# Kernel optimization log

Measured on AMD Instinct MI355X. Metric: run time of the kernel, lower is better.

The kernel has to match this reference:

```python
import jax, jax.numpy as jnp
import numpy as np

B, T, C, H, W = 8, 8, 32, 16, 28
NH, DK = 4, 8                 # n_head, d_k == d_v
RADIUS = [3, 3, 3, 3]
DILATION = [1, 3, 5, 7]
LN_EPS = 1e-5


def setup_inputs() -> dict:
    key = jax.random.key(0)
    ks = jax.random.split(key, 8)
    s = 1.0 / np.sqrt(C).astype(np.float32)
    return {
        "first": jax.random.normal(ks[0], (B, T, C, H, W), jnp.float32),
        "x": jax.random.normal(ks[1], (B, T, C, H, W), jnp.float32),
        "Wq": jax.random.normal(ks[2], (NH * DK, C), jnp.float32) * s,
        "Wk": jax.random.normal(ks[3], (NH * DK, C), jnp.float32) * s,
        "Wv": jax.random.normal(ks[4], (NH * DK, C), jnp.float32) * s,
        "Wo": jax.random.normal(ks[5], (C, NH * DK), jnp.float32) * s,
        "ln_gamma": 1.0 + 0.1 * jax.random.normal(ks[6], (DK, H, W), jnp.float32),
        "ln_beta": 0.1 * jax.random.normal(ks[7], (DK, H, W), jnp.float32),
    }


def _shift(x, dy, dx):
    # out[..., i, j] = x[..., i+dy, j+dx]; zero out-of-bounds. mask: (H, W) valid.
    h, w = x.shape[-2:]
    xs = jnp.roll(x, (-dy, -dx), axis=(-2, -1))
    mh = (jnp.arange(h) + dy >= 0) & (jnp.arange(h) + dy < h)
    mw = (jnp.arange(w) + dx >= 0) & (jnp.arange(w) + dx < w)
    m = mh[:, None] & mw[None, :]
    return jnp.where(m, xs, 0.0), m


def _head_attn(q, k, v, radius, dilation, scale):
    # q,k,v: (b,t,c,h,w). Returns softmaxed scores P (b,t,O*t,h,w) and
    # aggregation T (b,t,c,h,w). Aggregation uses RAW scaled scores (as the repo
    # does: spatial_temporal_aggregation receives M_A_i, not its softmax).
    b, t, c, h, w = q.shape
    scores, vals, masks = [], [], []
    for dy in range(-radius, radius + 1):
        for dx in range(-radius, radius + 1):
            ks, m = _shift(k, dy * dilation, dx * dilation)
            vs, _ = _shift(v, dy * dilation, dx * dilation)
            # score against all source frames s at the shifted spatial location
            scores.append(jnp.einsum('btchw,bschw->btshw', q, ks))
            vals.append(vs)
            masks.append(m)
    A = jnp.stack(scores, axis=2)                      # (b,t,O,s,h,w), O=(2r+1)^2
    M = jnp.stack(masks, axis=0)                       # (O,h,w)
    A = jnp.where(M[None, None, :, None], A / scale, -jnp.inf)
    O = A.shape[2]
    P = jax.nn.softmax(A.reshape(b, t, O * t, h, w), axis=2)
    Wm = jnp.where(M[None, None, :, None], A, 0.0)     # skip invalid (-inf) slots
    V = jnp.stack(vals, axis=0)                        # (O,b,s,c,h,w)
    Tout = jnp.einsum('btoshw,obschw->btchw', Wm, V)
    return P, Tout


def reference(first, x, Wq, Wk, Wv, Wo, ln_gamma, ln_beta):
    b, t, c, h, w = x.shape
    q = jnp.einsum('btchw,oc->btohw', first, Wq).reshape(b, t, NH, DK, h, w)
    k = jnp.einsum('btchw,oc->btohw', x, Wk).reshape(b, t, NH, DK, h, w)
    v = jnp.einsum('btchw,oc->btohw', x, Wv).reshape(b, t, NH, DK, h, w)
    scale = float(np.sqrt(C / NH))
    Ps, Ts = [], []
    for i in range(NH):
        qi = q[:, :, i]
        mu = jnp.mean(qi, axis=(2, 3, 4), keepdims=True)
        var = jnp.var(qi, axis=(2, 3, 4), keepdims=True)
        qi = (qi - mu) / jnp.sqrt(var + LN_EPS) * ln_gamma + ln_beta
        P, Ti = _head_attn(qi, k[:, :, i], v[:, :, i], RADIUS[i], DILATION[i], scale)
        Ps.append(P)
        Ts.append(Ti)
    M_S = jnp.max(jnp.concatenate(Ps, axis=2), axis=2)   # (b,t,h,w)
    M_T = jnp.concatenate(Ts, axis=2)                    # (b,t,NH*DK,h,w)
    out = jnp.einsum('btchw,oc->btohw', M_T, Wo) * M_S[:, :, None]
    return out
```

## Files before the change

kernel.cpp:

```cpp
#include <hip/hip_runtime.h>

#define Bc 8
#define Tc 8
#define Cc 32
#define Hc 16
#define Wc 28
#define NHc 4
#define DKc 8
#define HWc (Hc*Wc)
#define INV_SCALE 0.35355339059327373f
#define LN_EPSc 1e-5f

typedef _Float16 half8 __attribute__((ext_vector_type(8)));


__global__ __launch_bounds__(448) void qkv_ln_kernel(
    const float* __restrict__ first, const float* __restrict__ x,
    const float* __restrict__ Wq, const float* __restrict__ Wk,
    const float* __restrict__ Wv,
    const float* __restrict__ gamma, const float* __restrict__ beta,
    float4* __restrict__ Q, float* __restrict__ K, float* __restrict__ V)
{
    int blk  = blockIdx.x;
    int head = blk >> 6;
    int bt   = blk & 63;
    int t    = bt % Tc;
    int b    = bt / Tc;
    int tid  = threadIdx.x;

    const float* fp = first + (size_t)bt * Cc * HWc + tid;
    const float* xp = x     + (size_t)bt * Cc * HWc + tid;
    float fv[Cc], xv[Cc];
#pragma unroll
    for (int c = 0; c < Cc; ++c) { fv[c] = fp[c*HWc]; xv[c] = xp[c*HWc]; }

    float qv[DKc], kv[DKc], vv[DKc];
#pragma unroll
    for (int dk = 0; dk < DKc; ++dk) {
        int o = head*DKc + dk;
        float aq = 0.f, ak = 0.f, av = 0.f;
#pragma unroll
        for (int c = 0; c < Cc; ++c) {
            aq = fmaf(Wq[o*Cc+c], fv[c], aq);
            ak = fmaf(Wk[o*Cc+c], xv[c], ak);
            av = fmaf(Wv[o*Cc+c], xv[c], av);
        }
        qv[dk] = aq; kv[dk] = ak; vv[dk] = av;
    }

    int bh = b*NHc + head;
    float* kp = K + (((size_t)bh*Tc + t)*HWc + tid)*DKc;
    float* vp = V + (((size_t)bh*Tc + t)*HWc + tid)*DKc;
    *(float4*)(kp)   = make_float4(kv[0],kv[1],kv[2],kv[3]);
    *(float4*)(kp+4) = make_float4(kv[4],kv[5],kv[6],kv[7]);
    *(float4*)(vp)   = make_float4(vv[0],vv[1],vv[2],vv[3]);
    *(float4*)(vp+4) = make_float4(vv[4],vv[5],vv[6],vv[7]);

    float s1 = 0.f, s2 = 0.f;
#pragma unroll
    for (int dk = 0; dk < DKc; ++dk) { s1 += qv[dk]; s2 += qv[dk]*qv[dk]; }
#pragma unroll
    for (int off = 32; off >= 1; off >>= 1) {
        s1 += __shfl_down(s1, off, 64);
        s2 += __shfl_down(s2, off, 64);
    }
    __shared__ float r1[8], r2[8];
    int wid = tid >> 6, lane = tid & 63;
    if (lane == 0) { r1[wid] = s1; r2[wid] = s2; }
    __syncthreads();
    float S1 = 0.f, S2 = 0.f;
#pragma unroll
    for (int wv2 = 0; wv2 < 7; ++wv2) { S1 += r1[wv2]; S2 += r2[wv2]; }
    const float invN = 1.f / (float)(DKc * HWc);
    float mu   = S1 * invN;
    float var  = S2 * invN - mu*mu;
    float rstd = rsqrtf(var + LN_EPSc);

    float qn[DKc];
#pragma unroll
    for (int dk = 0; dk < DKc; ++dk) {
        float gg = gamma[dk*HWc + tid];
        float bb = beta [dk*HWc + tid];
        qn[dk] = ((qv[dk] - mu) * rstd * gg + bb) * INV_SCALE;
    }
    Q[(((size_t)bh*Tc + t)*2 + 0)*HWc + tid] = make_float4(qn[0],qn[1],qn[2],qn[3]);
    Q[(((size_t)bh*Tc + t)*2 + 1)*HWc + tid] = make_float4(qn[4],qn[5],qn[6],qn[7]);
}

__device__ __forceinline__ void attn_item(
    int bh, int dil, int s, int t0, int tid, int w, int h,
    const float4* __restrict__ sK0, const float4* __restrict__ sK1,
    const float4* __restrict__ sV0, const float4* __restrict__ sV1,
    const float4* __restrict__ Q,
    half8* __restrict__ Tpart, float2* __restrict__ LMpart)
{
    float4 q0[4], q1[4];
    const float4* qb = Q + (size_t)bh*Tc*2*HWc + tid;
#pragma unroll
    for (int j = 0; j < 4; ++j) {
        q0[j] = qb[((t0+j)*2+0)*HWc];
        q1[j] = qb[((t0+j)*2+1)*HWc];
    }

    float4 a0[4], a1[4];
    float l[4], m[4];
#pragma unroll
    for (int j = 0; j < 4; ++j) {
        a0[j] = make_float4(0.f,0.f,0.f,0.f);
        a1[j] = make_float4(0.f,0.f,0.f,0.f);
        l[j] = 0.f; m[j] = -1e30f;
    }

    for (int dy = -3; dy <= 3; ++dy) {
        int hy = h + dy*dil;
        if ((unsigned)hy >= (unsigned)Hc) continue;
        int rowbase = hy*Wc;
#pragma unroll
        for (int dx = -3; dx <= 3; ++dx) {
            int wx = w + dx*dil;
            int wcl = min(max(wx, 0), Wc-1);
            bool cv = (unsigned)wx < (unsigned)Wc;
            float bias = cv ? 0.f : -1e30f;
            float mask = cv ? 1.f : 0.f;
            int idx = rowbase + wcl;
            float4 k0 = sK0[idx], k1 = sK1[idx];
            float4 v0 = sV0[idx], v1 = sV1[idx];
#pragma unroll
            for (int j = 0; j < 4; ++j) {
                float sc = q0[j].x*k0.x + q0[j].y*k0.y + q0[j].z*k0.z + q0[j].w*k0.w
                         + q1[j].x*k1.x + q1[j].y*k1.y + q1[j].z*k1.z + q1[j].w*k1.w;
                float msc = sc + bias;
                m[j] = fmaxf(m[j], msc);
                l[j] += __expf(msc);
                float z = sc * mask;
                a0[j].x = fmaf(z, v0.x, a0[j].x);
                a0[j].y = fmaf(z, v0.y, a0[j].y);
                a0[j].z = fmaf(z, v0.z, a0[j].z);
                a0[j].w = fmaf(z, v0.w, a0[j].w);
                a1[j].x = fmaf(z, v1.x, a1[j].x);
                a1[j].y = fmaf(z, v1.y, a1[j].y);
                a1[j].z = fmaf(z, v1.z, a1[j].z);
                a1[j].w = fmaf(z, v1.w, a1[j].w);
            }
        }
    }

    half8*  tp  = Tpart  + (size_t)(bh*Tc + s)*Tc*HWc + tid;
    float2* lmp = LMpart + (size_t)(bh*Tc + s)*Tc*HWc + tid;
#pragma unroll
    for (int j = 0; j < 4; ++j) {
        half8 hv;
        hv[0] = (_Float16)a0[j].x; hv[1] = (_Float16)a0[j].y;
        hv[2] = (_Float16)a0[j].z; hv[3] = (_Float16)a0[j].w;
        hv[4] = (_Float16)a1[j].x; hv[5] = (_Float16)a1[j].y;
        hv[6] = (_Float16)a1[j].z; hv[7] = (_Float16)a1[j].w;
        tp [(t0+j)*HWc] = hv;
        lmp[(t0+j)*HWc] = make_float2(l[j], m[j]);
    }
}

__global__ __launch_bounds__(448, 2) void attn_kernel(
    const float4* __restrict__ Q, const float* __restrict__ K,
    const float* __restrict__ V,
    half8* __restrict__ Tpart, float2* __restrict__ LMpart)
{
    int blk = blockIdx.x;
    int g   = blk & 1;
    int s   = (blk >> 1) & 7;
    int ha  = (blk >> 4) & 1;
    int b   = blk >> 5;

    int bhA = b*NHc + ha;            int dilA = 2*ha + 1;
    int bhB = b*NHc + (3 - ha);      int dilB = 7 - 2*ha;

    int tid = threadIdx.x;
    int w = tid % Wc;
    int h = tid / Wc;

    __shared__ float4 sKA0[HWc], sKA1[HWc], sVA0[HWc], sVA1[HWc];
    __shared__ float4 sKB0[HWc], sKB1[HWc], sVB0[HWc], sVB1[HWc];

    {
        const float* kpA = K + ((size_t)bhA*Tc + s)*HWc*DKc;
        const float* vpA = V + ((size_t)bhA*Tc + s)*HWc*DKc;
        const float* kpB = K + ((size_t)bhB*Tc + s)*HWc*DKc;
        const float* vpB = V + ((size_t)bhB*Tc + s)*HWc*DKc;
        sKA0[tid] = *(const float4*)(kpA + tid*DKc);
        sKA1[tid] = *(const float4*)(kpA + tid*DKc + 4);
        sVA0[tid] = *(const float4*)(vpA + tid*DKc);
        sVA1[tid] = *(const float4*)(vpA + tid*DKc + 4);
        sKB0[tid] = *(const float4*)(kpB + tid*DKc);
        sKB1[tid] = *(const float4*)(kpB + tid*DKc + 4);
        sVB0[tid] = *(const float4*)(vpB + tid*DKc);
        sVB1[tid] = *(const float4*)(vpB + tid*DKc + 4);
    }
    __syncthreads();

    int t0 = g*4;
    attn_item(bhA, dilA, s, t0, tid, w, h, sKA0, sKA1, sVA0, sVA1, Q, Tpart, LMpart);
    attn_item(bhB, dilB, s, t0, tid, w, h, sKB0, sKB1, sVB0, sVB1, Q, Tpart, LMpart);
}

__global__ __launch_bounds__(448) void combine_kernel(
    const half8* __restrict__ Tpart, const float2* __restrict__ LMpart,
    float4* __restrict__ Tout, float* __restrict__ Mprob)
{
    int blk = blockIdx.x;
    int t   = blk & 7;
    int bh  = blk >> 3;
    int tid = threadIdx.x;

    float s0x=0.f,s0y=0.f,s0z=0.f,s0w=0.f;
    float s1x=0.f,s1y=0.f,s1z=0.f,s1w=0.f;
    float lsum = 0.f, mmax = -1e30f;
#pragma unroll
    for (int s = 0; s < Tc; ++s) {
        half8 u = Tpart[(size_t)((bh*Tc + s)*Tc + t)*HWc + tid];
        s0x += (float)u[0]; s0y += (float)u[1]; s0z += (float)u[2]; s0w += (float)u[3];
        s1x += (float)u[4]; s1y += (float)u[5]; s1z += (float)u[6]; s1w += (float)u[7];
        float2 lm = LMpart[(size_t)((bh*Tc + s)*Tc + t)*HWc + tid];
        lsum += lm.x; mmax = fmaxf(mmax, lm.y);
    }
    Tout[(size_t)((bh*Tc + t)*2 + 0)*HWc + tid] = make_float4(s0x,s0y,s0z,s0w);
    Tout[(size_t)((bh*Tc + t)*2 + 1)*HWc + tid] = make_float4(s1x,s1y,s1z,s1w);
    Mprob[(size_t)(bh*Tc + t)*HWc + tid] = __expf(mmax) / lsum;
}

__global__ __launch_bounds__(448) void outproj_kernel(
    const float4* __restrict__ Tout, const float* __restrict__ Mprob,
    const float* __restrict__ Wo, float* __restrict__ out)
{
    int blk = blockIdx.x;
    int og  = blk >> 6;
    int bt  = blk & 63;
    int b   = bt / Tc, t = bt % Tc;
    int tid = threadIdx.x;

    float mv[Cc];
    float MS = 0.f;
#pragma unroll
    for (int head = 0; head < NHc; ++head) {
        int bh = b*NHc + head;
        float4 u0 = Tout[(size_t)((bh*Tc + t)*2 + 0)*HWc + tid];
        float4 u1 = Tout[(size_t)((bh*Tc + t)*2 + 1)*HWc + tid];
        mv[head*8+0]=u0.x; mv[head*8+1]=u0.y; mv[head*8+2]=u0.z; mv[head*8+3]=u0.w;
        mv[head*8+4]=u1.x; mv[head*8+5]=u1.y; mv[head*8+6]=u1.z; mv[head*8+7]=u1.w;
        MS = fmaxf(MS, Mprob[(size_t)(bh*Tc + t)*HWc + tid]);
    }
#pragma unroll
    for (int i = 0; i < 8; ++i) {
        int o = og*8 + i;
        float acc = 0.f;
#pragma unroll
        for (int c = 0; c < Cc; ++c) acc = fmaf(Wo[o*Cc+c], mv[c], acc);
        out[((size_t)bt*Cc + o)*HWc + tid] = acc * MS;
    }
}

extern "C" void kernel_launch(void* const* d_in, const int* in_sizes, int n_in,
                              void* d_out, int out_size, void* d_ws, size_t ws_size,
                              hipStream_t stream) {
    const float* first = (const float*)d_in[0];
    const float* x     = (const float*)d_in[1];
    const float* Wq    = (const float*)d_in[2];
    const float* Wk    = (const float*)d_in[3];
    const float* Wv    = (const float*)d_in[4];
    const float* Wo    = (const float*)d_in[5];
    const float* g     = (const float*)d_in[6];
    const float* bta   = (const float*)d_in[7];
    float* out = (float*)d_out;

    float* ws = (float*)d_ws;
    const size_t N5 = (size_t)Bc*NHc*Tc*HWc*DKc;
    float4* Q   = (float4*)ws;
    float*  K   = ws +   N5;
    float*  V   = ws + 2*N5;
    float4* Tt  = (float4*)(ws + 3*N5);
    float*  Mp  = ws + 4*N5;
    half8*  Tp  = (half8*)(ws + 4*N5 + N5/8);
    float2* LMp = (float2*)(ws + 8*N5 + N5/8);

    qkv_ln_kernel <<<Bc*Tc*NHc, 448, 0, stream>>>(first, x, Wq, Wk, Wv, g, bta, Q, K, V);
    attn_kernel   <<<256,       448, 0, stream>>>(Q, K, V, Tp, LMp);
    combine_kernel<<<Bc*NHc*Tc, 448, 0, stream>>>(Tp, LMp, Tt, Mp);
    outproj_kernel<<<256,       448, 0, stream>>>(Tt, Mp, Wo, out);
}
```

Before: 123.3 us.

## Fuse all four stages into one persistent kernel with atomic grid barriers

Merges the QKV/layernorm, attention, combine and output-projection kernels into a single 256-block launch that separates the phases with software grid barriers built on a global atomic counter. The combine step is folded into the output projection, so the intermediate Tout and Mprob buffers are no longer written or read. This removes three kernel launch boundaries and one round trip through global memory. In exchange it requires all 256 blocks to be co-resident for the spin barrier to be safe, adds a memset launch, and adds barrier latency and redundant recombination, since each output block re-reduces all heads.

```diff
diff --git a/kernel.cpp b/kernel.cpp
--- a/kernel.cpp
+++ b/kernel.cpp
@@ -14,83 +14,22 @@
 typedef _Float16 half8 __attribute__((ext_vector_type(8)));
 
 
-__global__ __launch_bounds__(448) void qkv_ln_kernel(
-    const float* __restrict__ first, const float* __restrict__ x,
-    const float* __restrict__ Wq, const float* __restrict__ Wk,
-    const float* __restrict__ Wv,
-    const float* __restrict__ gamma, const float* __restrict__ beta,
-    float4* __restrict__ Q, float* __restrict__ K, float* __restrict__ V)
-{
-    int blk  = blockIdx.x;
-    int head = blk >> 6;
-    int bt   = blk & 63;
-    int t    = bt % Tc;
-    int b    = bt / Tc;
-    int tid  = threadIdx.x;
-
-    const float* fp = first + (size_t)bt * Cc * HWc + tid;
-    const float* xp = x     + (size_t)bt * Cc * HWc + tid;
-    float fv[Cc], xv[Cc];
-#pragma unroll
-    for (int c = 0; c < Cc; ++c) { fv[c] = fp[c*HWc]; xv[c] = xp[c*HWc]; }
-
-    float qv[DKc], kv[DKc], vv[DKc];
-#pragma unroll
-    for (int dk = 0; dk < DKc; ++dk) {
-        int o = head*DKc + dk;
-        float aq = 0.f, ak = 0.f, av = 0.f;
-#pragma unroll
-        for (int c = 0; c < Cc; ++c) {
-            aq = fmaf(Wq[o*Cc+c], fv[c], aq);
-            ak = fmaf(Wk[o*Cc+c], xv[c], ak);
-            av = fmaf(Wv[o*Cc+c], xv[c], av);
-        }
-        qv[dk] = aq; kv[dk] = ak; vv[dk] = av;
-    }
-
-    int bh = b*NHc + head;
-    float* kp = K + (((size_t)bh*Tc + t)*HWc + tid)*DKc;
-    float* vp = V + (((size_t)bh*Tc + t)*HWc + tid)*DKc;
-    *(float4*)(kp)   = make_float4(kv[0],kv[1],kv[2],kv[3]);
-    *(float4*)(kp+4) = make_float4(kv[4],kv[5],kv[6],kv[7]);
-    *(float4*)(vp)   = make_float4(vv[0],vv[1],vv[2],vv[3]);
-    *(float4*)(vp+4) = make_float4(vv[4],vv[5],vv[6],vv[7]);
-
-    float s1 = 0.f, s2 = 0.f;
-#pragma unroll
-    for (int dk = 0; dk < DKc; ++dk) { s1 += qv[dk]; s2 += qv[dk]*qv[dk]; }
-#pragma unroll
-    for (int off = 32; off >= 1; off >>= 1) {
-        s1 += __shfl_down(s1, off, 64);
-        s2 += __shfl_down(s2, off, 64);
-    }
-    __shared__ float r1[8], r2[8];
-    int wid = tid >> 6, lane = tid & 63;
-    if (lane == 0) { r1[wid] = s1; r2[wid] = s2; }
+__device__ __forceinline__ void gridbar(unsigned* cnt, unsigned target) {
     __syncthreads();
-    float S1 = 0.f, S2 = 0.f;
-#pragma unroll
-    for (int wv2 = 0; wv2 < 7; ++wv2) { S1 += r1[wv2]; S2 += r2[wv2]; }
-    const float invN = 1.f / (float)(DKc * HWc);
-    float mu   = S1 * invN;
-    float var  = S2 * invN - mu*mu;
-    float rstd = rsqrtf(var + LN_EPSc);
-
-    float qn[DKc];
-#pragma unroll
-    for (int dk = 0; dk < DKc; ++dk) {
-        float gg = gamma[dk*HWc + tid];
-        float bb = beta [dk*HWc + tid];
-        qn[dk] = ((qv[dk] - mu) * rstd * gg + bb) * INV_SCALE;
-    }
-    Q[(((size_t)bh*Tc + t)*2 + 0)*HWc + tid] = make_float4(qn[0],qn[1],qn[2],qn[3]);
-    Q[(((size_t)bh*Tc + t)*2 + 1)*HWc + tid] = make_float4(qn[4],qn[5],qn[6],qn[7]);
+    if (threadIdx.x == 0) {
+        __threadfence();
+        __hip_atomic_fetch_add(cnt, 1u, __ATOMIC_ACQ_REL, __HIP_MEMORY_SCOPE_AGENT);
+        while (__hip_atomic_load(cnt, __ATOMIC_ACQUIRE, __HIP_MEMORY_SCOPE_AGENT) < target)
+            __builtin_amdgcn_s_sleep(2);
+        __threadfence();
+    }
+    __syncthreads();
 }
 
 __device__ __forceinline__ void attn_item(
     int bh, int dil, int s, int t0, int tid, int w, int h,
-    const float4* __restrict__ sK0, const float4* __restrict__ sK1,
-    const float4* __restrict__ sV0, const float4* __restrict__ sV1,
+    const float4* sK0, const float4* sK1,
+    const float4* sV0, const float4* sV1,
     const float4* __restrict__ Q,
     half8* __restrict__ Tpart, float2* __restrict__ LMpart)
 {
@@ -159,28 +98,114 @@
     }
 }
 
-__global__ __launch_bounds__(448, 2) void attn_kernel(
-    const float4* __restrict__ Q, const float* __restrict__ K,
-    const float* __restrict__ V,
-    half8* __restrict__ Tpart, float2* __restrict__ LMpart)
+__global__ __launch_bounds__(448, 4) void fused_kernel(
+    const float* __restrict__ first, const float* __restrict__ x,
+    const float* __restrict__ Wq, const float* __restrict__ Wk,
+    const float* __restrict__ Wv, const float* __restrict__ Wo,
+    const float* __restrict__ gamma, const float* __restrict__ beta,
+    float* __restrict__ Qf, float* __restrict__ K, float* __restrict__ V,
+    half8* __restrict__ Tpart, float2* __restrict__ LMpart,
+    float* __restrict__ out, unsigned* __restrict__ cnt)
 {
     int blk = blockIdx.x;
-    int g   = blk & 1;
-    int s   = (blk >> 1) & 7;
-    int ha  = (blk >> 4) & 1;
-    int b   = blk >> 5;
-
-    int bhA = b*NHc + ha;            int dilA = 2*ha + 1;
-    int bhB = b*NHc + (3 - ha);      int dilB = 7 - 2*ha;
-
     int tid = threadIdx.x;
-    int w = tid % Wc;
-    int h = tid / Wc;
-
-    __shared__ float4 sKA0[HWc], sKA1[HWc], sVA0[HWc], sVA1[HWc];
-    __shared__ float4 sKB0[HWc], sKB1[HWc], sVB0[HWc], sVB1[HWc];
+
+    __shared__ float4 sbuf[8*HWc];
+    float* rbuf = (float*)sbuf;
 
     {
+        int head = blk >> 6;
+        int bt   = blk & 63;
+        int t    = bt & 7;
+        int b    = bt >> 3;
+
+        const float* fp = first + (size_t)bt * Cc * HWc + tid;
+        const float* xp = x     + (size_t)bt * Cc * HWc + tid;
+
+        float qv[DKc], kv[DKc], vv[DKc];
+#pragma unroll
+        for (int j = 0; j < DKc; ++j) { qv[j] = 0.f; kv[j] = 0.f; vv[j] = 0.f; }
+
+        for (int c0 = 0; c0 < Cc; c0 += 8) {
+            float f8[8], x8[8];
+#pragma unroll
+            for (int j = 0; j < 8; ++j) {
+                f8[j] = fp[(c0+j)*HWc];
+                x8[j] = xp[(c0+j)*HWc];
+            }
+#pragma unroll
+            for (int dk = 0; dk < DKc; ++dk) {
+                int o = head*DKc + dk;
+                const float* wq = Wq + o*Cc + c0;
+                const float* wk = Wk + o*Cc + c0;
+                const float* wv = Wv + o*Cc + c0;
+#pragma unroll
+                for (int j = 0; j < 8; ++j) {
+                    qv[dk] = fmaf(wq[j], f8[j], qv[dk]);
+                    kv[dk] = fmaf(wk[j], x8[j], kv[dk]);
+                    vv[dk] = fmaf(wv[j], x8[j], vv[dk]);
+                }
+            }
+        }
+
+        int bh = b*NHc + head;
+        float* kp = K + (((size_t)bh*Tc + t)*HWc + tid)*DKc;
+        float* vp = V + (((size_t)bh*Tc + t)*HWc + tid)*DKc;
+        *(float4*)(kp)   = make_float4(kv[0],kv[1],kv[2],kv[3]);
+        *(float4*)(kp+4) = make_float4(kv[4],kv[5],kv[6],kv[7]);
+        *(float4*)(vp)   = make_float4(vv[0],vv[1],vv[2],vv[3]);
+        *(float4*)(vp+4) = make_float4(vv[4],vv[5],vv[6],vv[7]);
+
+        float s1 = 0.f, s2 = 0.f;
+#pragma unroll
+        for (int dk = 0; dk < DKc; ++dk) { s1 += qv[dk]; s2 += qv[dk]*qv[dk]; }
+#pragma unroll
+        for (int off = 32; off >= 1; off >>= 1) {
+            s1 += __shfl_down(s1, off, 64);
+            s2 += __shfl_down(s2, off, 64);
+        }
+        int wid = tid >> 6, lane = tid & 63;
+        if (lane == 0) { rbuf[wid] = s1; rbuf[8+wid] = s2; }
+        __syncthreads();
+        float S1 = 0.f, S2 = 0.f;
+#pragma unroll
+        for (int wv2 = 0; wv2 < 7; ++wv2) { S1 += rbuf[wv2]; S2 += rbuf[8+wv2]; }
+        const float invN = 1.f / (float)(DKc * HWc);
+        float mu   = S1 * invN;
+        float var  = S2 * invN - mu*mu;
+        float rstd = rsqrtf(var + LN_EPSc);
+
+        float4* Q = (float4*)Qf;
+        float qn[DKc];
+#pragma unroll
+        for (int dk = 0; dk < DKc; ++dk) {
+            float gg = gamma[dk*HWc + tid];
+            float bb = beta [dk*HWc + tid];
+            qn[dk] = ((qv[dk] - mu) * rstd * gg + bb) * INV_SCALE;
+        }
+        Q[(((size_t)bh*Tc + t)*2 + 0)*HWc + tid] = make_float4(qn[0],qn[1],qn[2],qn[3]);
+        Q[(((size_t)bh*Tc + t)*2 + 1)*HWc + tid] = make_float4(qn[4],qn[5],qn[6],qn[7]);
+    }
+
+    gridbar(cnt, 256);
+
+    {
+        int g   = blk & 1;
+        int s   = (blk >> 1) & 7;
+        int ha  = (blk >> 4) & 1;
+        int b   = blk >> 5;
+
+        int bhA = b*NHc + ha;            int dilA = 2*ha + 1;
+        int bhB = b*NHc + (3 - ha);      int dilB = 7 - 2*ha;
+
+        int w = tid % Wc;
+        int h = tid / Wc;
+
+        float4* sKA0 = sbuf;            float4* sKA1 = sbuf + HWc;
+        float4* sVA0 = sbuf + 2*HWc;    float4* sVA1 = sbuf + 3*HWc;
+        float4* sKB0 = sbuf + 4*HWc;    float4* sKB1 = sbuf + 5*HWc;
+        float4* sVB0 = sbuf + 6*HWc;    float4* sVB1 = sbuf + 7*HWc;
+
         const float* kpA = K + ((size_t)bhA*Tc + s)*HWc*DKc;
         const float* vpA = V + ((size_t)bhA*Tc + s)*HWc*DKc;
         const float* kpB = K + ((size_t)bhB*Tc + s)*HWc*DKc;
@@ -193,67 +218,50 @@
         sKB1[tid] = *(const float4*)(kpB + tid*DKc + 4);
         sVB0[tid] = *(const float4*)(vpB + tid*DKc);
         sVB1[tid] = *(const float4*)(vpB + tid*DKc + 4);
-    }
-    __syncthreads();
-
-    int t0 = g*4;
-    attn_item(bhA, dilA, s, t0, tid, w, h, sKA0, sKA1, sVA0, sVA1, Q, Tpart, LMpart);
-    attn_item(bhB, dilB, s, t0, tid, w, h, sKB0, sKB1, sVB0, sVB1, Q, Tpart, LMpart);
-}
-
-__global__ __launch_bounds__(448) void combine_kernel(
-    const half8* __restrict__ Tpart, const float2* __restrict__ LMpart,
-    float4* __restrict__ Tout, float* __restrict__ Mprob)
-{
-    int blk = blockIdx.x;
-    int t   = blk & 7;
-    int bh  = blk >> 3;
-    int tid = threadIdx.x;
-
-    float s0x=0.f,s0y=0.f,s0z=0.f,s0w=0.f;
-    float s1x=0.f,s1y=0.f,s1z=0.f,s1w=0.f;
-    float lsum = 0.f, mmax = -1e30f;
-#pragma unroll
-    for (int s = 0; s < Tc; ++s) {
-        half8 u = Tpart[(size_t)((bh*Tc + s)*Tc + t)*HWc + tid];
-        s0x += (float)u[0]; s0y += (float)u[1]; s0z += (float)u[2]; s0w += (float)u[3];
-        s1x += (float)u[4]; s1y += (float)u[5]; s1z += (float)u[6]; s1w += (float)u[7];
-        float2 lm = LMpart[(size_t)((bh*Tc + s)*Tc + t)*HWc + tid];
-        lsum += lm.x; mmax = fmaxf(mmax, lm.y);
-    }
-    Tout[(size_t)((bh*Tc + t)*2 + 0)*HWc + tid] = make_float4(s0x,s0y,s0z,s0w);
-    Tout[(size_t)((bh*Tc + t)*2 + 1)*HWc + tid] = make_float4(s1x,s1y,s1z,s1w);
-    Mprob[(size_t)(bh*Tc + t)*HWc + tid] = __expf(mmax) / lsum;
-}
-
-__global__ __launch_bounds__(448) void outproj_kernel(
-    const float4* __restrict__ Tout, const float* __restrict__ Mprob,
-    const float* __restrict__ Wo, float* __restrict__ out)
-{
-    int blk = blockIdx.x;
-    int og  = blk >> 6;
-    int bt  = blk & 63;
-    int b   = bt / Tc, t = bt % Tc;
-    int tid = threadIdx.x;
-
-    float mv[Cc];
-    float MS = 0.f;
-#pragma unroll
-    for (int head = 0; head < NHc; ++head) {
-        int bh = b*NHc + head;
-        float4 u0 = Tout[(size_t)((bh*Tc + t)*2 + 0)*HWc + tid];
-        float4 u1 = Tout[(size_t)((bh*Tc + t)*2 + 1)*HWc + tid];
-        mv[head*8+0]=u0.x; mv[head*8+1]=u0.y; mv[head*8+2]=u0.z; mv[head*8+3]=u0.w;
-        mv[head*8+4]=u1.x; mv[head*8+5]=u1.y; mv[head*8+6]=u1.z; mv[head*8+7]=u1.w;
-        MS = fmaxf(MS, Mprob[(size_t)(bh*Tc + t)*HWc + tid]);
-    }
-#pragma unroll
-    for (int i = 0; i < 8; ++i) {
-        int o = og*8 + i;
-        float acc = 0.f;
-#pragma unroll
-        for (int c = 0; c < Cc; ++c) acc = fmaf(Wo[o*Cc+c], mv[c], acc);
-        out[((size_t)bt*Cc + o)*HWc + tid] = acc * MS;
+        __syncthreads();
+
+        int t0 = g*4;
+        const float4* Q = (const float4*)Qf;
+        attn_item(bhA, dilA, s, t0, tid, w, h, sKA0, sKA1, sVA0, sVA1, Q, Tpart, LMpart);
+        attn_item(bhB, dilB, s, t0, tid, w, h, sKB0, sKB1, sVB0, sVB1, Q, Tpart, LMpart);
+    }
+
+    gridbar(cnt, 512);
+
+    {
+        int og  = blk >> 6;
+        int bt  = blk & 63;
+        int b   = bt >> 3, t = bt & 7;
+
+        float mv[Cc];
+        float MS = 0.f;
+#pragma unroll
+        for (int head = 0; head < NHc; ++head) {
+            int bh = b*NHc + head;
+            float acc[DKc];
+#pragma unroll
+            for (int j = 0; j < DKc; ++j) acc[j] = 0.f;
+            float lsum = 0.f, mmax = -1e30f;
+#pragma unroll
+            for (int s = 0; s < Tc; ++s) {
+                half8 u = Tpart[(size_t)((bh*Tc + s)*Tc + t)*HWc + tid];
+#pragma unroll
+                for (int j = 0; j < DKc; ++j) acc[j] += (float)u[j];
+                float2 lm = LMpart[(size_t)((bh*Tc + s)*Tc + t)*HWc + tid];
+                lsum += lm.x; mmax = fmaxf(mmax, lm.y);
+            }
+#pragma unroll
+            for (int j = 0; j < DKc; ++j) mv[head*DKc + j] = acc[j];
+            MS = fmaxf(MS, __expf(mmax) / lsum);
+        }
+#pragma unroll
+        for (int i = 0; i < 8; ++i) {
+            int o = og*8 + i;
+            float a = 0.f;
+#pragma unroll
+            for (int c = 0; c < Cc; ++c) a = fmaf(Wo[o*Cc+c], mv[c], a);
+            out[((size_t)bt*Cc + o)*HWc + tid] = a * MS;
+        }
     }
 }
 
@@ -272,16 +280,14 @@
 
     float* ws = (float*)d_ws;
     const size_t N5 = (size_t)Bc*NHc*Tc*HWc*DKc;
-    float4* Q   = (float4*)ws;
-    float*  K   = ws +   N5;
-    float*  V   = ws + 2*N5;
-    float4* Tt  = (float4*)(ws + 3*N5);
-    float*  Mp  = ws + 4*N5;
-    half8*  Tp  = (half8*)(ws + 4*N5 + N5/8);
-    float2* LMp = (float2*)(ws + 8*N5 + N5/8);
-
-    qkv_ln_kernel <<<Bc*Tc*NHc, 448, 0, stream>>>(first, x, Wq, Wk, Wv, g, bta, Q, K, V);
-    attn_kernel   <<<256,       448, 0, stream>>>(Q, K, V, Tp, LMp);
-    combine_kernel<<<Bc*NHc*Tc, 448, 0, stream>>>(Tp, LMp, Tt, Mp);
-    outproj_kernel<<<256,       448, 0, stream>>>(Tt, Mp, Wo, out);
-}
+    float*    Q   = ws;
+    float*    K   = ws +   N5;
+    float*    V   = ws + 2*N5;
+    half8*    Tp  = (half8*)(ws + 3*N5);
+    float2*   LMp = (float2*)(ws + 7*N5);
+    unsigned* cnt = (unsigned*)(ws + 9*N5);
+
+    hipMemsetAsync(cnt, 0, sizeof(unsigned), stream);
+    fused_kernel<<<256, 448, 0, stream>>>(first, x, Wq, Wk, Wv, Wo, g, bta,
+                                          Q, K, V, Tp, LMp, out, cnt);
+}
```

Measured after the change: 222.7 us. 80.6% more time.
